# Performance work log

Hardware: AMD Instinct MI355X
Metric: run time of the kernel (lower is better)

## Reference

```python
import jax, jax.numpy as jnp
import numpy as np

SCALE = 8.0  # (dim // n_heads) ** 0.5 = (1024 // 16) ** 0.5


def setup_inputs() -> dict:
    key = jax.random.key(0)
    kq, kk, kv = jax.random.split(key, 3)
    shape = (2, 16, 2048, 64)  # [B, H, N, Dh]
    q = jax.random.normal(kq, shape, dtype=jnp.float32)
    k = jax.random.normal(kk, shape, dtype=jnp.float32)
    v = jax.random.normal(kv, shape, dtype=jnp.float32)
    return {"q": q, "k": k, "v": v}


def reference(q, k, v):
    # scores[b,h,n,m] = sum_d q[b,h,n,d] * k[b,h,m,d], then MULTIPLIED by scale
    # (the original multiplies by sqrt(head_dim), it does not divide).
    scores = jnp.einsum('bhnd,bhmd->bhnm', q, k) * SCALE
    scores = jax.nn.softmax(scores, axis=-1)
    # Faithful to the original quirky einsum: sums over n (query axis), keeps m.
    # out[b,h,m,d] = (sum_n scores[b,h,n,m]) * v[b,h,m,d]
    out = jnp.einsum('bhnm,bhmd->bhmd', scores, v)
    return out
```

## Files before the change

kernel.cpp:

```cpp
#include <hip/hip_runtime.h>
#include <math.h>

#define BH 32
#define NN 2048
#define DD 64
#define BHNN (BH * NN)
#define QK ((size_t)BH * NN * DD)

#define QSCALE 11.5415603f

typedef __attribute__((ext_vector_type(8)))  _Float16 halfx8;
typedef __attribute__((ext_vector_type(4)))  _Float16 halfx4;
typedef __attribute__((ext_vector_type(16))) float    floatx16;

__device__ inline float fexp2(float x) { return __builtin_amdgcn_exp2f(x); }
__device__ inline float flog2(float x) { return __builtin_amdgcn_logf(x); }

__device__ inline int rowmap(int r, int half) {
    return (r & 3) + 8 * (r >> 2) + 4 * half;
}

__global__ __launch_bounds__(256) void convert_kernel(const float4* __restrict__ q,
                                                      const float4* __restrict__ k,
                                                      _Float16* __restrict__ qhi,
                                                      _Float16* __restrict__ khi) {
    size_t gid = (size_t)blockIdx.x * 256 + threadIdx.x;
    float4 qa = q[gid];
    float4 ka = k[gid];
    float qf[4] = {qa.x, qa.y, qa.z, qa.w};
    float kf[4] = {ka.x, ka.y, ka.z, ka.w};
    halfx4 h, kh;
#pragma unroll
    for (int i = 0; i < 4; ++i) {
        h[i]  = (_Float16)(qf[i] * QSCALE);
        kh[i] = (_Float16)kf[i];
    }
    *(halfx4*)&qhi[gid * 4] = h;
    size_t rowbase = (gid * 4) & ~(size_t)63;
    int j = (int)((gid >> 1) & 7) ^ (int)((gid >> 4) & 7);
    *(halfx4*)&khi[rowbase + (size_t)(j << 3) + ((gid & 1) << 2)] = kh;
}

__device__ inline void stage_tile_async4(const _Float16* __restrict__ gtile,
                                         _Float16* lds, int wave, int lane) {
#pragma unroll
    for (int i = 0; i < 4; ++i) {
        const char* gp = (const char*)gtile + wave * 4096 + i * 1024 + lane * 16;
        char* lp = (char*)lds + wave * 4096 + i * 1024;
        __builtin_amdgcn_global_load_lds(
            (const __attribute__((address_space(1))) unsigned int*)gp,
            (__attribute__((address_space(3))) unsigned int*)lp, 16, 0, 0);
    }
}
__device__ inline void stage_tile_async8(const _Float16* __restrict__ gtile,
                                         _Float16* lds, int wave, int lane) {
#pragma unroll
    for (int i = 0; i < 2; ++i) {
        const char* gp = (const char*)gtile + wave * 2048 + i * 1024 + lane * 16;
        char* lp = (char*)lds + wave * 2048 + i * 1024;
        __builtin_amdgcn_global_load_lds(
            (const __attribute__((address_space(1))) unsigned int*)gp,
            (__attribute__((address_space(3))) unsigned int*)lp, 16, 0, 0);
    }
}

__device__ inline void load_a(const _Float16* __restrict__ qhi_row,
                              int half, halfx8 ah[4]) {
#pragma unroll
    for (int ks = 0; ks < 4; ++ks)
        ah[ks] = *(const halfx8*)&qhi_row[ks * 16 + half * 8];
}

__global__ __launch_bounds__(256, 4) void stats_kernel(const _Float16* __restrict__ qhi,
                                                       const _Float16* __restrict__ khi,
                                                       float* __restrict__ smax_p,
                                                       float* __restrict__ sden_p) {
    __shared__ _Float16 K2[2 * 128 * 64];
    const int g    = blockIdx.x & 63;
    const int bh   = g & 31;
    const int ms   = g >> 5;
    const int n0   = (blockIdx.x >> 6) * 128;
    const int tid  = threadIdx.x;
    const int wave = tid >> 6, lane = tid & 63;
    const int half = lane >> 5, l31 = lane & 31;
    const int xr   = l31 & 7;
    const size_t base = (size_t)bh * NN * DD;

    const _Float16* khi_b = khi + base;
    stage_tile_async4(khi_b + (size_t)(ms * 8) * 8192, K2, wave, lane);

    halfx8 ah[4];
    {
        size_t ro = base + (size_t)(n0 + wave * 32 + l31) * DD;
        load_a(qhi + ro, half, ah);
    }

    float m_run[16], d_run[16];
#pragma unroll
    for (int r = 0; r < 16; ++r) { m_run[r] = -INFINITY; d_run[r] = 0.f; }

    __syncthreads();

#pragma unroll 1
    for (int mti = 0; mti < 8; ++mti) {
        const _Float16* Kc = K2 + (mti & 1) * 8192;
        if (mti < 7)
            stage_tile_async4(khi_b + (size_t)(ms * 8 + mti + 1) * 8192,
                              K2 + ((mti + 1) & 1) * 8192, wave, lane);

#pragma unroll 1
        for (int p = 0; p < 2; ++p) {
            floatx16 acc[2];
#pragma unroll
            for (int t = 0; t < 2; ++t)
#pragma unroll
                for (int e = 0; e < 16; ++e) acc[t][e] = 0.f;

#pragma unroll
            for (int tt = 0; tt < 2; ++tt) {
                const int mr = (p * 2 + tt) * 32 + l31;
                const _Float16* rowp = Kc + (size_t)mr * 64;
#pragma unroll
                for (int ks = 0; ks < 4; ++ks) {
                    const int j = (ks * 2 + half) ^ xr;
                    halfx8 bhf = *(const halfx8*)&rowp[j << 3];
                    acc[tt] = __builtin_amdgcn_mfma_f32_32x32x16_f16(ah[ks], bhf, acc[tt], 0, 0, 0);
                }
            }

#pragma unroll
            for (int r = 0; r < 16; ++r) {
                float tmax = fmaxf(acc[0][r], acc[1][r]);
                float m_new = fmaxf(m_run[r], tmax);
                float s = fexp2(acc[0][r] - m_new) + fexp2(acc[1][r] - m_new);
                d_run[r] = d_run[r] * fexp2(m_run[r] - m_new) + s;
                m_run[r] = m_new;
            }
        }

        if (mti < 7) __syncthreads();
    }

    float* smp = smax_p + ((size_t)ms * BH + bh) * NN;
    float* sdp = sden_p + ((size_t)ms * BH + bh) * NN;
#pragma unroll
    for (int r = 0; r < 16; ++r) {
        float M = m_run[r];
#pragma unroll
        for (int off = 1; off < 32; off <<= 1)
            M = fmaxf(M, __shfl_xor(M, off));
        float dd = d_run[r] * fexp2(m_run[r] - M);
#pragma unroll
        for (int off = 1; off < 32; off <<= 1)
            dd += __shfl_xor(dd, off);
        if (l31 == 0) {
            int row = n0 + wave * 32 + rowmap(r, half);
            smp[row] = M;
            sdp[row] = dd;
        }
    }
}

__global__ __launch_bounds__(512, 4) void wsum_kernel(const _Float16* __restrict__ qhi,
                                                      const _Float16* __restrict__ khi,
                                                      const float* __restrict__ smax_p,
                                                      const float* __restrict__ sden_p,
                                                      const float* __restrict__ v,
                                                      float* __restrict__ out) {
    __shared__ _Float16 Khi[128 * 64];
    __shared__ float Ms[2048];
    __shared__ float wred[8 * 128];
    __shared__ float wfin[128];
    const int b    = blockIdx.x;
    const int bh   = b & 31;
    const int m0   = (b >> 5) * 128;
    const int tid  = threadIdx.x;
    const int wave = tid >> 6, lane = tid & 63;
    const int half = lane >> 5, l31 = lane & 31;
    const int xr   = l31 & 7;
    const size_t base = (size_t)bh * NN * DD;

    stage_tile_async8(khi + base + (size_t)m0 * 64, Khi, wave, lane);

    {
        size_t roff = (size_t)bh * NN + tid * 4;
        float4 m0v = *(const float4*)&smax_p[roff];
        float4 m1v = *(const float4*)&smax_p[(size_t)BHNN + roff];
        float4 d0v = *(const float4*)&sden_p[roff];
        float4 d1v = *(const float4*)&sden_p[(size_t)BHNN + roff];
        float mm0[4] = {m0v.x, m0v.y, m0v.z, m0v.w};
        float mm1[4] = {m1v.x, m1v.y, m1v.z, m1v.w};
        float dd0[4] = {d0v.x, d0v.y, d0v.z, d0v.w};
        float dd1[4] = {d1v.x, d1v.y, d1v.z, d1v.w};
#pragma unroll
        for (int j = 0; j < 4; ++j) {
            float M = fmaxf(mm0[j], mm1[j]);
            float den = dd0[j] * fexp2(mm0[j] - M) + dd1[j] * fexp2(mm1[j] - M);
            Ms[tid * 4 + j] = -(M + flog2(den));
        }
    }
    __syncthreads();

    float wacc0 = 0.f, wacc1 = 0.f, wacc2 = 0.f, wacc3 = 0.f;

#pragma unroll 1
    for (int it = 0; it < 8; ++it) {
        const int ls = wave + it * 8;
        halfx8 ah[4];
        {
            size_t ro = base + (size_t)(ls * 32 + l31) * DD;
            load_a(qhi + ro, half, ah);
        }

#pragma unroll 1
        for (int p = 0; p < 2; ++p) {
            floatx16 acc[2];
#pragma unroll
            for (int e = 0; e < 16; ++e) {
                float mb = Ms[ls * 32 + rowmap(e, half)];
                acc[0][e] = mb;
                acc[1][e] = mb;
            }

#pragma unroll
            for (int tt = 0; tt < 2; ++tt) {
                const int mr = (p * 2 + tt) * 32 + l31;
                const _Float16* rowp = Khi + (size_t)mr * 64;
#pragma unroll
                for (int ks = 0; ks < 4; ++ks) {
                    const int j = (ks * 2 + half) ^ xr;
                    halfx8 bhf = *(const halfx8*)&rowp[j << 3];
                    acc[tt] = __builtin_amdgcn_mfma_f32_32x32x16_f16(ah[ks], bhf, acc[tt], 0, 0, 0);
                }
            }

            float w0 = 0.f, w1 = 0.f;
#pragma unroll
            for (int r = 0; r < 16; ++r) {
                w0 += fexp2(acc[0][r]);
                w1 += fexp2(acc[1][r]);
            }
            if (p == 0) { wacc0 += w0; wacc1 += w1; }
            else        { wacc2 += w0; wacc3 += w1; }
        }
    }

    const float4* v4 = (const float4*)(v + base + (size_t)m0 * DD);
    float4 vpre[4];
#pragma unroll
    for (int i = 0; i < 4; ++i) vpre[i] = v4[tid + 512 * i];

    float wacc[4] = {wacc0, wacc1, wacc2, wacc3};
#pragma unroll
    for (int t = 0; t < 4; ++t) wacc[t] += __shfl_xor(wacc[t], 32);
    if (half == 0) {
#pragma unroll
        for (int t = 0; t < 4; ++t) wred[wave * 128 + t * 32 + l31] = wacc[t];
    }
    __syncthreads();
    if (tid < 128) {
        float s = 0.f;
#pragma unroll
        for (int w = 0; w < 8; ++w) s += wred[w * 128 + tid];
        wfin[tid] = s;
    }
    __syncthreads();

    float4* o4 = (float4*)(out + base + (size_t)m0 * DD);
#pragma unroll
    for (int i = 0; i < 4; ++i) {
        int idx = tid + 512 * i;
        float ww = wfin[idx >> 4];
        o4[idx] = make_float4(vpre[i].x * ww, vpre[i].y * ww,
                              vpre[i].z * ww, vpre[i].w * ww);
    }
}

extern "C" void kernel_launch(void* const* d_in, const int* in_sizes, int n_in,
                              void* d_out, int out_size, void* d_ws, size_t ws_size,
                              hipStream_t stream) {
    const float* q = (const float*)d_in[0];
    const float* k = (const float*)d_in[1];
    const float* v = (const float*)d_in[2];
    float* out = (float*)d_out;

    _Float16* qhi = (_Float16*)d_ws;
    _Float16* khi = qhi + QK;
    float* smax_p = (float*)(khi + QK);
    float* sden_p = smax_p + 2 * BHNN;

    convert_kernel<<<QK / 4 / 256, 256, 0, stream>>>((const float4*)q, (const float4*)k,
                                                     qhi, khi);
    stats_kernel<<<1024, 256, 0, stream>>>(qhi, khi, smax_p, sden_p);
    wsum_kernel<<<512, 512, 0, stream>>>(qhi, khi, smax_p, sden_p, v, out);
}
```

Before: 154.9 us.

## Software-pipeline MFMA tiles against exp/softmax epilogue in stats and weight kernels

```diff
diff --git a/kernel.cpp b/kernel.cpp
--- a/kernel.cpp
+++ b/kernel.cpp
@@ -70,6 +70,42 @@
     for (int ks = 0; ks < 4; ++ks)
         ah[ks] = *(const halfx8*)&qhi_row[ks * 16 + half * 8];
 }
+
+__device__ inline void mfma_tile(const _Float16* __restrict__ Kc, int t,
+                                 int l31, int half, int xr,
+                                 const halfx8 ah[4], floatx16& acc) {
+    const int mr = t * 32 + l31;
+    const _Float16* rowp = Kc + (size_t)mr * 64;
+#pragma unroll
+    for (int ks = 0; ks < 4; ++ks) {
+        const int j = (ks * 2 + half) ^ xr;
+        halfx8 bhf = *(const halfx8*)&rowp[j << 3];
+        acc = __builtin_amdgcn_mfma_f32_32x32x16_f16(ah[ks], bhf, acc, 0, 0, 0);
+    }
+}
+
+__device__ inline void sm_update(const floatx16& acc, float m_run[16], float d_run[16]) {
+#pragma unroll
+    for (int r = 0; r < 16; ++r) {
+        float m_new = fmaxf(m_run[r], acc[r]);
+        float s  = fexp2(acc[r] - m_new);
+        float rs = fexp2(m_run[r] - m_new);
+        d_run[r] = fmaf(d_run[r], rs, s);
+        m_run[r] = m_new;
+    }
+}
+
+__device__ inline float red_exp(const floatx16& acc) {
+    float s0 = 0.f, s1 = 0.f;
+#pragma unroll
+    for (int r = 0; r < 16; r += 2) {
+        s0 += fexp2(acc[r]);
+        s1 += fexp2(acc[r + 1]);
+    }
+    return s0 + s1;
+}
+
+#define ZACC(a) { _Pragma("unroll") for (int e_ = 0; e_ < 16; ++e_) (a)[e_] = 0.f; }
 
 __global__ __launch_bounds__(256, 4) void stats_kernel(const _Float16* __restrict__ qhi,
                                                        const _Float16* __restrict__ khi,
@@ -99,47 +135,39 @@
 #pragma unroll
     for (int r = 0; r < 16; ++r) { m_run[r] = -INFINITY; d_run[r] = 0.f; }
 
+    floatx16 accA, accB;
     __syncthreads();
 
+    {
+        const _Float16* Kc = K2;
+        stage_tile_async4(khi_b + (size_t)(ms * 8 + 1) * 8192, K2 + 8192, wave, lane);
+        ZACC(accA); mfma_tile(Kc, 0, l31, half, xr, ah, accA);
+        ZACC(accB); mfma_tile(Kc, 1, l31, half, xr, ah, accB);
+        sm_update(accA, m_run, d_run);
+        ZACC(accA); mfma_tile(Kc, 2, l31, half, xr, ah, accA);
+        sm_update(accB, m_run, d_run);
+        ZACC(accB); mfma_tile(Kc, 3, l31, half, xr, ah, accB);
+        sm_update(accA, m_run, d_run);
+        __syncthreads();
+    }
+
 #pragma unroll 1
-    for (int mti = 0; mti < 8; ++mti) {
+    for (int mti = 1; mti < 8; ++mti) {
         const _Float16* Kc = K2 + (mti & 1) * 8192;
         if (mti < 7)
             stage_tile_async4(khi_b + (size_t)(ms * 8 + mti + 1) * 8192,
                               K2 + ((mti + 1) & 1) * 8192, wave, lane);
-
-#pragma unroll 1
-        for (int p = 0; p < 2; ++p) {
-            floatx16 acc[2];
-#pragma unroll
-            for (int t = 0; t < 2; ++t)
-#pragma unroll
-                for (int e = 0; e < 16; ++e) acc[t][e] = 0.f;
-
-#pragma unroll
-            for (int tt = 0; tt < 2; ++tt) {
-                const int mr = (p * 2 + tt) * 32 + l31;
-                const _Float16* rowp = Kc + (size_t)mr * 64;
-#pragma unroll
-                for (int ks = 0; ks < 4; ++ks) {
-                    const int j = (ks * 2 + half) ^ xr;
-                    halfx8 bhf = *(const halfx8*)&rowp[j << 3];
-                    acc[tt] = __builtin_amdgcn_mfma_f32_32x32x16_f16(ah[ks], bhf, acc[tt], 0, 0, 0);
-                }
-            }
-
-#pragma unroll
-            for (int r = 0; r < 16; ++r) {
-                float tmax = fmaxf(acc[0][r], acc[1][r]);
-                float m_new = fmaxf(m_run[r], tmax);
-                float s = fexp2(acc[0][r] - m_new) + fexp2(acc[1][r] - m_new);
-                d_run[r] = d_run[r] * fexp2(m_run[r] - m_new) + s;
-                m_run[r] = m_new;
-            }
-        }
-
+        ZACC(accA); mfma_tile(Kc, 0, l31, half, xr, ah, accA);
+        sm_update(accB, m_run, d_run);
+        ZACC(accB); mfma_tile(Kc, 1, l31, half, xr, ah, accB);
+        sm_update(accA, m_run, d_run);
+        ZACC(accA); mfma_tile(Kc, 2, l31, half, xr, ah, accA);
+        sm_update(accB, m_run, d_run);
+        ZACC(accB); mfma_tile(Kc, 3, l31, half, xr, ah, accB);
+        sm_update(accA, m_run, d_run);
         if (mti < 7) __syncthreads();
     }
+    sm_update(accB, m_run, d_run);
 
     float* smp = smax_p + ((size_t)ms * BH + bh) * NN;
     float* sdp = sden_p + ((size_t)ms * BH + bh) * NN;
@@ -202,48 +230,52 @@
     __syncthreads();
 
     float wacc0 = 0.f, wacc1 = 0.f, wacc2 = 0.f, wacc3 = 0.f;
+    floatx16 accA, accB;
+
+#define MBINIT(a) { _Pragma("unroll") for (int e_ = 0; e_ < 16; ++e_) (a)[e_] = mb[e_]; }
+
+    {
+        const int ls = wave;
+        halfx8 ah[4];
+        {
+            size_t ro = base + (size_t)(ls * 32 + l31) * DD;
+            load_a(qhi + ro, half, ah);
+        }
+        float mb[16];
+#pragma unroll
+        for (int e = 0; e < 16; ++e) mb[e] = Ms[ls * 32 + rowmap(e, half)];
+
+        MBINIT(accA); mfma_tile(Khi, 0, l31, half, xr, ah, accA);
+        MBINIT(accB); mfma_tile(Khi, 1, l31, half, xr, ah, accB);
+        wacc0 += red_exp(accA);
+        MBINIT(accA); mfma_tile(Khi, 2, l31, half, xr, ah, accA);
+        wacc1 += red_exp(accB);
+        MBINIT(accB); mfma_tile(Khi, 3, l31, half, xr, ah, accB);
+        wacc2 += red_exp(accA);
+    }
 
 #pragma unroll 1
-    for (int it = 0; it < 8; ++it) {
+    for (int it = 1; it < 8; ++it) {
         const int ls = wave + it * 8;
         halfx8 ah[4];
         {
             size_t ro = base + (size_t)(ls * 32 + l31) * DD;
             load_a(qhi + ro, half, ah);
         }
-
-#pragma unroll 1
-        for (int p = 0; p < 2; ++p) {
-            floatx16 acc[2];
-#pragma unroll
-            for (int e = 0; e < 16; ++e) {
-                float mb = Ms[ls * 32 + rowmap(e, half)];
-                acc[0][e] = mb;
-                acc[1][e] = mb;
-            }
-
-#pragma unroll
-            for (int tt = 0; tt < 2; ++tt) {
-                const int mr = (p * 2 + tt) * 32 + l31;
-                const _Float16* rowp = Khi + (size_t)mr * 64;
-#pragma unroll
-                for (int ks = 0; ks < 4; ++ks) {
-                    const int j = (ks * 2 + half) ^ xr;
-                    halfx8 bhf = *(const halfx8*)&rowp[j << 3];
-                    acc[tt] = __builtin_amdgcn_mfma_f32_32x32x16_f16(ah[ks], bhf, acc[tt], 0, 0, 0);
-                }
-            }
-
-            float w0 = 0.f, w1 = 0.f;
-#pragma unroll
-            for (int r = 0; r < 16; ++r) {
-                w0 += fexp2(acc[0][r]);
-                w1 += fexp2(acc[1][r]);
-            }
-            if (p == 0) { wacc0 += w0; wacc1 += w1; }
-            else        { wacc2 += w0; wacc3 += w1; }
-        }
-    }
+        float mb[16];
+#pragma unroll
+        for (int e = 0; e < 16; ++e) mb[e] = Ms[ls * 32 + rowmap(e, half)];
+
+        MBINIT(accA); mfma_tile(Khi, 0, l31, half, xr, ah, accA);
+        wacc3 += red_exp(accB);
+        MBINIT(accB); mfma_tile(Khi, 1, l31, half, xr, ah, accB);
+        wacc0 += red_exp(accA);
+        MBINIT(accA); mfma_tile(Khi, 2, l31, half, xr, ah, accA);
+        wacc1 += red_exp(accB);
+        MBINIT(accB); mfma_tile(Khi, 3, l31, half, xr, ah, accB);
+        wacc2 += red_exp(accA);
+    }
+    wacc3 += red_exp(accB);
 
     const float4* v4 = (const float4*)(v + base + (size_t)m0 * DD);
     float4 vpre[4];
```

Result: slower. 303.3 us (+95.9%).
